# Kernel optimization log

Hardware: AMD Instinct MI355X
Metric: run time of the kernel (lower is better)

Reference implementation:

```python
import jax, jax.numpy as jnp
import numpy as np

H = 8          # num_att_heads
D_IN = 64      # input_size
D_H = 32       # lin_hidden
B = 32         # batch
N = 512        # target_dim (num nodes)
NEG = -9.0e15  # masked-score fill from the torch source
LRELU_SLOPE = 0.2


def setup_inputs() -> dict:
    key = jax.random.key(0)
    ks = jax.random.split(key, 14)
    g = lambda k, shape, s=0.1: jax.random.normal(k, shape, dtype=jnp.float32) * s
    return {
        "inputs": jax.random.normal(ks[0], (B, N, D_IN), dtype=jnp.float32),
        "hidden": jax.random.normal(ks[1], (B, N, D_H), dtype=jnp.float32),
        # per-head projection [H, D_IN, D_H] (att_hidden=0 -> attention uses h)
        "linear": g(ks[2], (H, D_IN, D_H)),
        "bias": jnp.zeros((1, D_H), dtype=jnp.float32),
        "att_src": g(ks[3], (H, D_H)),  # attention_vect_src squeezed
        "att_tar": g(ks[4], (H, D_H)),  # attention_vect_tar squeezed
        # GRU-style gate weights (nn.Linear equivalents, stored as [in, out])
        "W_hr": g(ks[5], (D_H, D_H)),
        "W_hi": g(ks[6], (D_H, D_H)),
        "W_hm": g(ks[7], (D_H, D_H)),
        "W_ir": g(ks[8], (D_IN, D_H)), "b_ir": jnp.zeros((D_H,), jnp.float32),
        "W_ii": g(ks[9], (D_IN, D_H)), "b_ii": jnp.zeros((D_H,), jnp.float32),
        "W_in": g(ks[10], (D_IN, D_H)), "b_in": jnp.zeros((D_H,), jnp.float32),
    }


def reference(inputs, hidden, linear, bias, att_src, att_tar,
              W_hr, W_hi, W_hm, W_ir, b_ir, W_ii, b_ii, W_in, b_in):
    # dropout p=0.0 -> identity (inference math)
    # per-head linear projection: h[h,b,n,k]
    h = jnp.einsum('bnd,hdk->hbnk', inputs, linear)
    # additive attention scores (att_hidden == 0 -> h_att = h)
    e_src = jnp.einsum('hbnk,hk->hbn', h, att_src)   # [H,B,N]
    e_tar = jnp.einsum('hbnk,hk->hbn', h, att_tar)   # [H,B,N]
    # score[h,b,i,j] = e_tar[h,b,i] + e_src[h,b,j]  (h_tar + h_src^T)
    score = e_tar[..., :, None] + e_src[..., None, :]
    score = jax.nn.leaky_relu(score, negative_slope=LRELU_SLOPE)
    # adj = ones - eye: mask self-edges only
    n = inputs.shape[1]
    eye = jnp.eye(n, dtype=bool)
    score = jnp.where(eye, jnp.float32(NEG), score)
    att = jax.nn.softmax(score, axis=-1)             # [H,B,N,N]
    # weighted aggregation then mean over heads
    msgs = jnp.einsum('hbij,hbjk->bik', att, h) / jnp.float32(h.shape[0])
    msgs = jnp.tanh(msgs + bias)                     # [B,N,D_H]
    # GRU-style gated update
    m = jax.nn.sigmoid(inputs @ W_ir + b_ir + msgs @ W_hr)
    i = jax.nn.sigmoid(inputs @ W_ii + b_ii + msgs @ W_hi)
    nn_ = jnp.tanh(inputs @ W_in + b_in + m * (msgs @ W_hm))
    new_hidden = i * nn_ + (1.0 - i) * hidden
    return new_hidden
```

## Files before the change

### kernel.cpp

```cpp
#include <hip/hip_runtime.h>

#define NN 512
#define DIN 64
#define DH 32
#define HSTR 520

typedef __attribute__((ext_vector_type(8))) short short8;
typedef __attribute__((ext_vector_type(4))) short short4v;
typedef __attribute__((ext_vector_type(4))) float f32x4;

__device__ __forceinline__ float bf2f(unsigned short u) {
    return __uint_as_float(((unsigned)u) << 16);
}
__device__ __forceinline__ unsigned short f2bf(float x) {
    unsigned u = __float_as_uint(x);
    u += 0x7FFF + ((u >> 16) & 1);
    return (unsigned short)(u >> 16);
}

__global__ __launch_bounds__(512) void attn_kernel(
    const float* __restrict__ in_g,
    const float* __restrict__ lin_g,
    const float* __restrict__ asrc_g,
    const float* __restrict__ atar_g,
    float* __restrict__ msgs8)
{
    __shared__ unsigned short h_t[DH * HSTR];
    __shared__ float s_arr[NN], e1s[NN], e2s[NN];
    __shared__ float cng[NN], e1t[NN], e2t[NN];
    __shared__ float dinv[NN];

    const int t = threadIdx.x;
    const int lane = t & 63, wv = t >> 6;
    const int l15 = lane & 15, quad = lane >> 4;
    const int hIdx = blockIdx.x & 7, bIdx = blockIdx.x >> 3;

    const float as_lo = asrc_g[hIdx * 32 + l15];
    const float as_hi = asrc_g[hIdx * 32 + l15 + 16];
    const float at_lo = atar_g[hIdx * 32 + l15];
    const float at_hi = atar_g[hIdx * 32 + l15 + 16];

    short8 bfrag[2][2];
    {
        const float* lp = lin_g + hIdx * (DIN * DH);
        for (int nt = 0; nt < 2; ++nt)
            for (int ks = 0; ks < 2; ++ks)
                #pragma unroll
                for (int j = 0; j < 8; ++j)
                    bfrag[nt][ks][j] = (short)f2bf(lp[(ks * 32 + quad * 8 + j) * DH + l15 + nt * 16]);
    }
    const float* xb = in_g + (size_t)bIdx * (NN * DIN);
    for (int mi = 0; mi < 4; ++mi) {
        int mt = wv * 4 + mi;
        int row = mt * 16 + l15;
        const float* rp = xb + row * DIN + quad * 8;
        f32x4 x0 = *((const f32x4*)rp);
        f32x4 x1 = *((const f32x4*)(rp + 4));
        f32x4 x2 = *((const f32x4*)(rp + 32));
        f32x4 x3 = *((const f32x4*)(rp + 36));
        short8 a0, a1;
        #pragma unroll
        for (int j = 0; j < 4; ++j) {
            a0[j]     = (short)f2bf(x0[j]);
            a0[4 + j] = (short)f2bf(x1[j]);
            a1[j]     = (short)f2bf(x2[j]);
            a1[4 + j] = (short)f2bf(x3[j]);
        }
        f32x4 c0 = {0.f, 0.f, 0.f, 0.f}, c1 = {0.f, 0.f, 0.f, 0.f};
        c0 = __builtin_amdgcn_mfma_f32_16x16x32_bf16(a0, bfrag[0][0], c0, 0, 0, 0);
        c0 = __builtin_amdgcn_mfma_f32_16x16x32_bf16(a1, bfrag[0][1], c0, 0, 0, 0);
        c1 = __builtin_amdgcn_mfma_f32_16x16x32_bf16(a0, bfrag[1][0], c1, 0, 0, 0);
        c1 = __builtin_amdgcn_mfma_f32_16x16x32_bf16(a1, bfrag[1][1], c1, 0, 0, 0);
        float ps[4], pt[4];
        #pragma unroll
        for (int r = 0; r < 4; ++r) {
            int m = mt * 16 + quad * 4 + r;
            h_t[l15 * HSTR + m]        = f2bf(c0[r]);
            h_t[(l15 + 16) * HSTR + m] = f2bf(c1[r]);
            ps[r] = c0[r] * as_lo + c1[r] * as_hi;
            pt[r] = c0[r] * at_lo + c1[r] * at_hi;
        }
        #pragma unroll
        for (int off = 1; off <= 8; off <<= 1) {
            #pragma unroll
            for (int r = 0; r < 4; ++r) {
                ps[r] += __shfl_xor(ps[r], off, 64);
                pt[r] += __shfl_xor(pt[r], off, 64);
            }
        }
        if (l15 < 4) {
            int r = l15;
            int m = mt * 16 + quad * 4 + r;
            float s = ps[r], tt = pt[r];
            s_arr[m] = s;
            e1s[m] = expf(s);   e2s[m] = expf(0.2f * s);
            cng[m] = -tt;
            e1t[m] = expf(tt);  e2t[m] = expf(0.2f * tt);
        }
    }
    __syncthreads();

    float cn[4], t1[4], t2[4];
    int iR[4];
    #pragma unroll
    for (int rt = 0; rt < 4; ++rt) {
        int rw = (wv * 4 + rt) * 16 + l15;
        iR[rt] = rw;
        cn[rt] = cng[rw]; t1[rt] = e1t[rw]; t2[rt] = e2t[rw];
    }
    f32x4 acc[4][2];
    float dacc[4];
    #pragma unroll
    for (int rt = 0; rt < 4; ++rt) {
        acc[rt][0] = (f32x4){0.f, 0.f, 0.f, 0.f};
        acc[rt][1] = (f32x4){0.f, 0.f, 0.f, 0.f};
        dacc[rt] = 0.f;
    }

    for (int kb = 0; kb < 16; ++kb) {
        const int j0 = kb * 32 + quad * 8;
        f32x4 sv0 = *(const f32x4*)&s_arr[j0], sv1 = *(const f32x4*)&s_arr[j0 + 4];
        f32x4 ev0 = *(const f32x4*)&e1s[j0],   ev1 = *(const f32x4*)&e1s[j0 + 4];
        f32x4 fv0 = *(const f32x4*)&e2s[j0],   fv1 = *(const f32x4*)&e2s[j0 + 4];
        short8 b0 = *(const short8*)&h_t[l15 * HSTR + j0];
        short8 b1 = *(const short8*)&h_t[(l15 + 16) * HSTR + j0];
        #pragma unroll
        for (int rt = 0; rt < 4; ++rt) {
            const bool selfkb = (kb == ((wv * 4 + rt) >> 1));
            float w8[8];
            #pragma unroll
            for (int jj = 0; jj < 8; ++jj) {
                float sj = (jj < 4) ? sv0[jj & 3] : sv1[jj & 3];
                float e1 = (jj < 4) ? ev0[jj & 3] : ev1[jj & 3];
                float e2 = (jj < 4) ? fv0[jj & 3] : fv1[jj & 3];
                float w = (sj > cn[rt]) ? t1[rt] * e1 : t2[rt] * e2;
                if (selfkb && (j0 + jj == iR[rt])) w = 0.f;
                dacc[rt] += w;
                w8[jj] = w;
            }
            union { unsigned u[4]; short8 s8; } au;
            #pragma unroll
            for (int pp = 0; pp < 4; ++pp) {
                unsigned lo = __float_as_uint(w8[2 * pp])     + 0x8000u;
                unsigned hi = __float_as_uint(w8[2 * pp + 1]) + 0x8000u;
                au.u[pp] = (lo >> 16) | (hi & 0xffff0000u);
            }
            acc[rt][0] = __builtin_amdgcn_mfma_f32_16x16x32_bf16(au.s8, b0, acc[rt][0], 0, 0, 0);
            acc[rt][1] = __builtin_amdgcn_mfma_f32_16x16x32_bf16(au.s8, b1, acc[rt][1], 0, 0, 0);
        }
    }

    #pragma unroll
    for (int rt = 0; rt < 4; ++rt) {
        float D = dacc[rt];
        D += __shfl_xor(D, 16, 64);
        D += __shfl_xor(D, 32, 64);
        if (quad == 0) dinv[iR[rt]] = 0.125f / D;
    }

    float* mbase = msgs8 + (size_t)blockIdx.x * (NN * DH);
    #pragma unroll
    for (int rt = 0; rt < 4; ++rt) {
        #pragma unroll
        for (int half = 0; half < 2; ++half) {
            #pragma unroll
            for (int r = 0; r < 4; ++r) {
                int row = (wv * 4 + rt) * 16 + quad * 4 + r;
                mbase[row * DH + half * 16 + l15] = acc[rt][half][r] * dinv[row];
            }
        }
    }
}

__global__ __launch_bounds__(256) void gru_kernel(
    const float* __restrict__ in_g,
    const float* __restrict__ hid_g,
    const float* __restrict__ bias_g,
    const float* __restrict__ Whr, const float* __restrict__ Whi,
    const float* __restrict__ Whm,
    const float* __restrict__ Wir, const float* __restrict__ bir,
    const float* __restrict__ Wii, const float* __restrict__ bii,
    const float* __restrict__ Win, const float* __restrict__ bin_,
    const float* __restrict__ msgs8,
    float* __restrict__ out_g)
{
    __shared__ float xs[64 * 100];
    __shared__ unsigned short WtL[3 * 32 * 100];

    const int t = threadIdx.x;
    const int rowbase = blockIdx.x * 64;
    const int bslice = blockIdx.x >> 3;
    const int r0 = (blockIdx.x & 7) * 64;

    for (int idx = t; idx < 1024; idx += 256) {
        int fi = idx * 4;
        int row = fi >> 6, d = fi & 63;
        f32x4 v = *(const f32x4*)&in_g[(size_t)(rowbase + row) * 64 + d];
        *(f32x4*)&xs[row * 100 + d] = v;
    }
    for (int idx = t; idx < 2048; idx += 256) {
        int row = idx >> 5, k2 = idx & 31;
        size_t base = (size_t)bslice * (8 * NN * DH) + (size_t)(r0 + row) * DH + k2;
        float s = 0.f;
        #pragma unroll
        for (int h = 0; h < 8; ++h) s += msgs8[base + (size_t)h * (NN * DH)];
        xs[row * 100 + 64 + k2] = tanhf(s + bias_g[k2]);
    }
    for (int idx = t; idx < 9216; idx += 256) {
        int g = idx / 3072, rem = idx % 3072;
        int d = rem >> 5, k2 = rem & 31;
        float v;
        if (g == 0) v = (d < 64) ? Wir[d * 32 + k2] : Whr[(d - 64) * 32 + k2];
        else if (g == 1) v = (d < 64) ? Wii[d * 32 + k2] : Whi[(d - 64) * 32 + k2];
        else v = (d < 64) ? Win[d * 32 + k2] : Whm[(d - 64) * 32 + k2];
        WtL[(g * 32 + k2) * 100 + d] = f2bf(v);
    }
    __syncthreads();

    const int k = t & 31, rg = t >> 5;
    const unsigned short* wp0 = &WtL[(0 * 32 + k) * 100];
    const unsigned short* wp1 = &WtL[(1 * 32 + k) * 100];
    const unsigned short* wp2 = &WtL[(2 * 32 + k) * 100];

    float pr[8], pi[8], xn[8], hm[8];
    #pragma unroll
    for (int r = 0; r < 8; ++r) { pr[r] = 0.f; pi[r] = 0.f; xn[r] = 0.f; hm[r] = 0.f; }

    for (int d0 = 0; d0 < 64; d0 += 4) {
        short4v wr4 = *(const short4v*)&wp0[d0];
        short4v wi4 = *(const short4v*)&wp1[d0];
        short4v wn4 = *(const short4v*)&wp2[d0];
        float wr[4], wi[4], wn[4];
        #pragma unroll
        for (int jj = 0; jj < 4; ++jj) {
            wr[jj] = bf2f((unsigned short)wr4[jj]);
            wi[jj] = bf2f((unsigned short)wi4[jj]);
            wn[jj] = bf2f((unsigned short)wn4[jj]);
        }
        #pragma unroll
        for (int r = 0; r < 8; ++r) {
            f32x4 xv = *(const f32x4*)&xs[(rg * 8 + r) * 100 + d0];
            #pragma unroll
            for (int jj = 0; jj < 4; ++jj) {
                pr[r] += xv[jj] * wr[jj];
                pi[r] += xv[jj] * wi[jj];
                xn[r] += xv[jj] * wn[jj];
            }
        }
    }
    for (int d0 = 64; d0 < 96; d0 += 4) {
        short4v wr4 = *(const short4v*)&wp0[d0];
        short4v wi4 = *(const short4v*)&wp1[d0];
        short4v wn4 = *(const short4v*)&wp2[d0];
        float wr[4], wi[4], wn[4];
        #pragma unroll
        for (int jj = 0; jj < 4; ++jj) {
            wr[jj] = bf2f((unsigned short)wr4[jj]);
            wi[jj] = bf2f((unsigned short)wi4[jj]);
            wn[jj] = bf2f((unsigned short)wn4[jj]);
        }
        #pragma unroll
        for (int r = 0; r < 8; ++r) {
            f32x4 xv = *(const f32x4*)&xs[(rg * 8 + r) * 100 + d0];
            #pragma unroll
            for (int jj = 0; jj < 4; ++jj) {
                pr[r] += xv[jj] * wr[jj];
                pi[r] += xv[jj] * wi[jj];
                hm[r] += xv[jj] * wn[jj];
            }
        }
    }

    const float bir_k = bir[k], bii_k = bii[k], bin_k = bin_[k];
    #pragma unroll
    for (int r = 0; r < 8; ++r) {
        int row = rowbase + rg * 8 + r;
        float m  = 1.f / (1.f + expf(-(pr[r] + bir_k)));
        float ig = 1.f / (1.f + expf(-(pi[r] + bii_k)));
        float nn = tanhf(xn[r] + bin_k + m * hm[r]);
        float ho = hid_g[(size_t)row * 32 + k];
        out_g[(size_t)row * 32 + k] = ig * nn + (1.f - ig) * ho;
    }
}

extern "C" void kernel_launch(void* const* d_in, const int* in_sizes, int n_in,
                              void* d_out, int out_size, void* d_ws, size_t ws_size,
                              hipStream_t stream)
{
    const float* inputs = (const float*)d_in[0];
    const float* hidden = (const float*)d_in[1];
    const float* linear = (const float*)d_in[2];
    const float* bias   = (const float*)d_in[3];
    const float* asrc   = (const float*)d_in[4];
    const float* atar   = (const float*)d_in[5];
    const float* Whr    = (const float*)d_in[6];
    const float* Whi    = (const float*)d_in[7];
    const float* Whm    = (const float*)d_in[8];
    const float* Wir    = (const float*)d_in[9];
    const float* bir    = (const float*)d_in[10];
    const float* Wii    = (const float*)d_in[11];
    const float* bii    = (const float*)d_in[12];
    const float* Win    = (const float*)d_in[13];
    const float* bin_   = (const float*)d_in[14];

    float* msgs8 = (float*)d_ws;
    attn_kernel<<<dim3(256), dim3(512), 0, stream>>>(inputs, linear, asrc, atar, msgs8);
    gru_kernel<<<dim3(256), dim3(256), 0, stream>>>(inputs, hidden, bias,
                                                    Whr, Whi, Whm,
                                                    Wir, bir, Wii, bii, Win, bin_,
                                                    msgs8, (float*)d_out);
}
```

Before: 133.4 us.

## Split attention key range across two blocks and combine partial sums in GRU

The attention kernel now launches 512 blocks, each handling half of the source-node (key) range for one head and batch. Each block writes unnormalised numerators and partial denominators, and the GRU kernel sums the two halves and normalises them. Attention scores are computed directly from inputs using a folded linear·att vector, so full scores are available without the full h projection. The goal is higher occupancy across the CUs. The cost is double the workspace traffic for numerators, redundant per-row target-score computation in both blocks, and extra combine work in the GRU kernel.

Result: slower. 167.5 us (+25.5%).

```diff
diff --git a/kernel.cpp b/kernel.cpp
--- a/kernel.cpp
+++ b/kernel.cpp
@@ -3,7 +3,7 @@
 #define NN 512
 #define DIN 64
 #define DH 32
-#define HSTR 520
+#define HT 264
 
 typedef __attribute__((ext_vector_type(8))) short short8;
 typedef __attribute__((ext_vector_type(4))) short short4v;
@@ -23,22 +23,52 @@
     const float* __restrict__ lin_g,
     const float* __restrict__ asrc_g,
     const float* __restrict__ atar_g,
-    float* __restrict__ msgs8)
+    float* __restrict__ numer,
+    float* __restrict__ denom)
 {
-    __shared__ unsigned short h_t[DH * HSTR];
-    __shared__ float s_arr[NN], e1s[NN], e2s[NN];
+    __shared__ unsigned short h_t[DH * HT];
+    __shared__ float wsv[DIN], wtv[DIN];
+    __shared__ float s_arr[256], e1s[256], e2s[256];
     __shared__ float cng[NN], e1t[NN], e2t[NN];
-    __shared__ float dinv[NN];
 
     const int t = threadIdx.x;
     const int lane = t & 63, wv = t >> 6;
     const int l15 = lane & 15, quad = lane >> 4;
-    const int hIdx = blockIdx.x & 7, bIdx = blockIdx.x >> 3;
-
-    const float as_lo = asrc_g[hIdx * 32 + l15];
-    const float as_hi = asrc_g[hIdx * 32 + l15 + 16];
-    const float at_lo = atar_g[hIdx * 32 + l15];
-    const float at_hi = atar_g[hIdx * 32 + l15 + 16];
+    const int jh   = blockIdx.x & 1;
+    const int hIdx = (blockIdx.x >> 1) & 7;
+    const int bIdx = blockIdx.x >> 4;
+    const int slice = blockIdx.x;
+
+    if (t < 128) {
+        int d = t & 63;
+        const float* av = (t < 64) ? (asrc_g + hIdx * 32) : (atar_g + hIdx * 32);
+        const float* lp = lin_g + hIdx * (DIN * DH) + d * DH;
+        float a = 0.f;
+        #pragma unroll
+        for (int k = 0; k < 32; ++k) a += lp[k] * av[k];
+        if (t < 64) wsv[d] = a; else wtv[d] = a;
+    }
+    __syncthreads();
+
+    const float* xb = in_g + (size_t)bIdx * (NN * DIN);
+    {
+        int r = t;
+        const float* xr = xb + r * DIN;
+        float ds = 0.f, dt = 0.f;
+        for (int d0 = 0; d0 < DIN; d0 += 4) {
+            f32x4 xv = *(const f32x4*)(xr + d0);
+            #pragma unroll
+            for (int j = 0; j < 4; ++j) {
+                ds += xv[j] * wsv[d0 + j];
+                dt += xv[j] * wtv[d0 + j];
+            }
+        }
+        cng[r] = -dt; e1t[r] = expf(dt); e2t[r] = expf(0.2f * dt);
+        int rl = r - jh * 256;
+        if ((unsigned)rl < 256u) {
+            s_arr[rl] = ds; e1s[rl] = expf(ds); e2s[rl] = expf(0.2f * ds);
+        }
+    }
 
     short8 bfrag[2][2];
     {
@@ -49,10 +79,9 @@
                 for (int j = 0; j < 8; ++j)
                     bfrag[nt][ks][j] = (short)f2bf(lp[(ks * 32 + quad * 8 + j) * DH + l15 + nt * 16]);
     }
-    const float* xb = in_g + (size_t)bIdx * (NN * DIN);
-    for (int mi = 0; mi < 4; ++mi) {
-        int mt = wv * 4 + mi;
-        int row = mt * 16 + l15;
+    for (int mi = 0; mi < 2; ++mi) {
+        int mt = wv * 2 + mi;
+        int row = jh * 256 + mt * 16 + l15;
         const float* rp = xb + row * DIN + quad * 8;
         f32x4 x0 = *((const f32x4*)rp);
         f32x4 x1 = *((const f32x4*)(rp + 4));
@@ -71,42 +100,22 @@
         c0 = __builtin_amdgcn_mfma_f32_16x16x32_bf16(a1, bfrag[0][1], c0, 0, 0, 0);
         c1 = __builtin_amdgcn_mfma_f32_16x16x32_bf16(a0, bfrag[1][0], c1, 0, 0, 0);
         c1 = __builtin_amdgcn_mfma_f32_16x16x32_bf16(a1, bfrag[1][1], c1, 0, 0, 0);
-        float ps[4], pt[4];
         #pragma unroll
         for (int r = 0; r < 4; ++r) {
-            int m = mt * 16 + quad * 4 + r;
-            h_t[l15 * HSTR + m]        = f2bf(c0[r]);
-            h_t[(l15 + 16) * HSTR + m] = f2bf(c1[r]);
-            ps[r] = c0[r] * as_lo + c1[r] * as_hi;
-            pt[r] = c0[r] * at_lo + c1[r] * at_hi;
-        }
-        #pragma unroll
-        for (int off = 1; off <= 8; off <<= 1) {
-            #pragma unroll
-            for (int r = 0; r < 4; ++r) {
-                ps[r] += __shfl_xor(ps[r], off, 64);
-                pt[r] += __shfl_xor(pt[r], off, 64);
-            }
-        }
-        if (l15 < 4) {
-            int r = l15;
-            int m = mt * 16 + quad * 4 + r;
-            float s = ps[r], tt = pt[r];
-            s_arr[m] = s;
-            e1s[m] = expf(s);   e2s[m] = expf(0.2f * s);
-            cng[m] = -tt;
-            e1t[m] = expf(tt);  e2t[m] = expf(0.2f * tt);
+            int mloc = mt * 16 + quad * 4 + r;
+            h_t[l15 * HT + mloc]        = f2bf(c0[r]);
+            h_t[(l15 + 16) * HT + mloc] = f2bf(c1[r]);
         }
     }
     __syncthreads();
 
-    float cn[4], t1[4], t2[4];
-    int iR[4];
+    float cn[4], t1v[4], t2v[4];
+    int iR[4], iRl[4];
     #pragma unroll
     for (int rt = 0; rt < 4; ++rt) {
         int rw = (wv * 4 + rt) * 16 + l15;
-        iR[rt] = rw;
-        cn[rt] = cng[rw]; t1[rt] = e1t[rw]; t2[rt] = e2t[rw];
+        iR[rt] = rw; iRl[rt] = rw - jh * 256;
+        cn[rt] = cng[rw]; t1v[rt] = e1t[rw]; t2v[rt] = e2t[rw];
     }
     f32x4 acc[4][2];
     float dacc[4];
@@ -117,24 +126,24 @@
         dacc[rt] = 0.f;
     }
 
-    for (int kb = 0; kb < 16; ++kb) {
+    for (int kb = 0; kb < 8; ++kb) {
         const int j0 = kb * 32 + quad * 8;
         f32x4 sv0 = *(const f32x4*)&s_arr[j0], sv1 = *(const f32x4*)&s_arr[j0 + 4];
         f32x4 ev0 = *(const f32x4*)&e1s[j0],   ev1 = *(const f32x4*)&e1s[j0 + 4];
         f32x4 fv0 = *(const f32x4*)&e2s[j0],   fv1 = *(const f32x4*)&e2s[j0 + 4];
-        short8 b0 = *(const short8*)&h_t[l15 * HSTR + j0];
-        short8 b1 = *(const short8*)&h_t[(l15 + 16) * HSTR + j0];
+        short8 b0 = *(const short8*)&h_t[l15 * HT + j0];
+        short8 b1 = *(const short8*)&h_t[(l15 + 16) * HT + j0];
         #pragma unroll
         for (int rt = 0; rt < 4; ++rt) {
-            const bool selfkb = (kb == ((wv * 4 + rt) >> 1));
+            const bool selfkb = ((iRl[rt] >> 5) == kb);
             float w8[8];
             #pragma unroll
             for (int jj = 0; jj < 8; ++jj) {
                 float sj = (jj < 4) ? sv0[jj & 3] : sv1[jj & 3];
                 float e1 = (jj < 4) ? ev0[jj & 3] : ev1[jj & 3];
                 float e2 = (jj < 4) ? fv0[jj & 3] : fv1[jj & 3];
-                float w = (sj > cn[rt]) ? t1[rt] * e1 : t2[rt] * e2;
-                if (selfkb && (j0 + jj == iR[rt])) w = 0.f;
+                float w = (sj > cn[rt]) ? t1v[rt] * e1 : t2v[rt] * e2;
+                if (selfkb && (j0 + jj == iRl[rt])) w = 0.f;
                 dacc[rt] += w;
                 w8[jj] = w;
             }
@@ -155,10 +164,10 @@
         float D = dacc[rt];
         D += __shfl_xor(D, 16, 64);
         D += __shfl_xor(D, 32, 64);
-        if (quad == 0) dinv[iR[rt]] = 0.125f / D;
-    }
-
-    float* mbase = msgs8 + (size_t)blockIdx.x * (NN * DH);
+        if (quad == 0) denom[(size_t)slice * NN + iR[rt]] = D;
+    }
+
+    float* nb = numer + (size_t)slice * (NN * DH);
     #pragma unroll
     for (int rt = 0; rt < 4; ++rt) {
         #pragma unroll
@@ -166,7 +175,7 @@
             #pragma unroll
             for (int r = 0; r < 4; ++r) {
                 int row = (wv * 4 + rt) * 16 + quad * 4 + r;
-                mbase[row * DH + half * 16 + l15] = acc[rt][half][r] * dinv[row];
+                nb[row * DH + half * 16 + l15] = acc[rt][half][r];
             }
         }
     }
@@ -181,11 +190,13 @@
     const float* __restrict__ Wir, const float* __restrict__ bir,
     const float* __restrict__ Wii, const float* __restrict__ bii,
     const float* __restrict__ Win, const float* __restrict__ bin_,
-    const float* __restrict__ msgs8,
+    const float* __restrict__ numer,
+    const float* __restrict__ denom,
     float* __restrict__ out_g)
 {
     __shared__ float xs[64 * 100];
     __shared__ unsigned short WtL[3 * 32 * 100];
+    __shared__ float Dl[64 * 8];
 
     const int t = threadIdx.x;
     const int rowbase = blockIdx.x * 64;
@@ -198,13 +209,12 @@
         f32x4 v = *(const f32x4*)&in_g[(size_t)(rowbase + row) * 64 + d];
         *(f32x4*)&xs[row * 100 + d] = v;
     }
-    for (int idx = t; idx < 2048; idx += 256) {
-        int row = idx >> 5, k2 = idx & 31;
-        size_t base = (size_t)bslice * (8 * NN * DH) + (size_t)(r0 + row) * DH + k2;
-        float s = 0.f;
-        #pragma unroll
-        for (int h = 0; h < 8; ++h) s += msgs8[base + (size_t)h * (NN * DH)];
-        xs[row * 100 + 64 + k2] = tanhf(s + bias_g[k2]);
+    for (int idx = t; idx < 512; idx += 256) {
+        int row = idx >> 3, h = idx & 7;
+        int sl0 = (bslice * 8 + h) * 2;
+        float D0 = denom[(size_t)sl0 * NN + (r0 + row)];
+        float D1 = denom[(size_t)(sl0 + 1) * NN + (r0 + row)];
+        Dl[row * 8 + h] = 0.125f / (D0 + D1);
     }
     for (int idx = t; idx < 9216; idx += 256) {
         int g = idx / 3072, rem = idx % 3072;
@@ -214,6 +224,17 @@
         else if (g == 1) v = (d < 64) ? Wii[d * 32 + k2] : Whi[(d - 64) * 32 + k2];
         else v = (d < 64) ? Win[d * 32 + k2] : Whm[(d - 64) * 32 + k2];
         WtL[(g * 32 + k2) * 100 + d] = f2bf(v);
+    }
+    __syncthreads();
+    for (int idx = t; idx < 2048; idx += 256) {
+        int row = idx >> 5, k2 = idx & 31;
+        float ssum = 0.f;
+        #pragma unroll
+        for (int h = 0; h < 8; ++h) {
+            size_t a0 = ((size_t)(bslice * 8 + h) * 2) * (NN * DH) + (size_t)(r0 + row) * DH + k2;
+            ssum += (numer[a0] + numer[a0 + (size_t)NN * DH]) * Dl[row * 8 + h];
+        }
+        xs[row * 100 + 64 + k2] = tanhf(ssum + bias_g[k2]);
     }
     __syncthreads();
 
@@ -303,10 +324,12 @@
     const float* Win    = (const float*)d_in[13];
     const float* bin_   = (const float*)d_in[14];
 
-    float* msgs8 = (float*)d_ws;
-    attn_kernel<<<dim3(256), dim3(512), 0, stream>>>(inputs, linear, asrc, atar, msgs8);
+    float* numer = (float*)d_ws;
+    float* denom = numer + (size_t)512 * NN * DH;
+    attn_kernel<<<dim3(512), dim3(512), 0, stream>>>(inputs, linear, asrc, atar,
+                                                     numer, denom);
     gru_kernel<<<dim3(256), dim3(256), 0, stream>>>(inputs, hidden, bias,
                                                     Whr, Whi, Whm,
                                                     Wir, bir, Wii, bii, Win, bin_,
-                                                    msgs8, (float*)d_out);
-}
+                                                    numer, denom, (float*)d_out);
+}
```
